# Kernel tuning notes

Measured on AMD Instinct MI355X. Metric: run time of the kernel, lower is better.

## Reference

```python
import jax, jax.numpy as jnp
import numpy as np

N = 50000
E = 800000
F_IN = 128
H = 64
C = 10
BN_EPS = 1e-5


def _glorot(key, shape):
    fan_in = shape[0]
    return jax.random.normal(key, shape, dtype=jnp.float32) / jnp.sqrt(jnp.float32(fan_in))


def setup_inputs() -> dict:
    key = jax.random.key(0)
    ks = jax.random.split(key, 16)
    inp = {
        "x": jax.random.normal(ks[0], (N, F_IN), dtype=jnp.float32),
        "edge_index": jax.random.randint(ks[1], (2, E), 0, N, dtype=jnp.int64),
    }
    # GINConv layer params: eps (train_eps=True, init 0), 2-layer MLP, BN affine
    dims = [(F_IN, H), (H, H), (H, H)]
    for i, (din, dout) in enumerate(dims, start=1):
        k1, k2 = jax.random.split(ks[1 + i], 2)
        inp[f"eps{i}"] = jnp.float32(0.0)
        inp[f"w{i}a"] = _glorot(k1, (din, H))
        inp[f"b{i}a"] = jnp.zeros((H,), jnp.float32)
        inp[f"w{i}b"] = _glorot(k2, (H, H))
        inp[f"b{i}b"] = jnp.zeros((H,), jnp.float32)
        inp[f"g{i}"] = jnp.ones((H,), jnp.float32)
        inp[f"be{i}"] = jnp.zeros((H,), jnp.float32)
    inp["lin_w"] = _glorot(ks[10], (H, C))
    inp["lin_b"] = jnp.zeros((C,), jnp.float32)
    return inp


def _gin_conv(x, src, dst, eps, wa, ba, wb, bb, g, be):
    # sum-aggregate neighbor features: scatter-add x[src] into dst rows
    agg = jax.ops.segment_sum(x[src], dst, num_segments=N)
    h = (1.0 + eps) * x + agg
    # MLP: Linear-ReLU-Linear-ReLU-BatchNorm1d (training-mode batch stats)
    h = jax.nn.relu(h @ wa + ba)
    h = jax.nn.relu(h @ wb + bb)
    mean = jnp.mean(h, axis=0)
    var = jnp.var(h, axis=0)
    return (h - mean) * jax.lax.rsqrt(var + BN_EPS) * g + be


def reference(x, edge_index,
              eps1, w1a, b1a, w1b, b1b, g1, be1,
              eps2, w2a, b2a, w2b, b2b, g2, be2,
              eps3, w3a, b3a, w3b, b3b, g3, be3,
              lin_w, lin_b):
    src, dst = edge_index[0], edge_index[1]
    h = jax.nn.relu(_gin_conv(x, src, dst, eps1, w1a, b1a, w1b, b1b, g1, be1))
    h = jax.nn.relu(_gin_conv(h, src, dst, eps2, w2a, b2a, w2b, b2b, g2, be2))
    h = jax.nn.relu(_gin_conv(h, src, dst, eps3, w3a, b3a, w3b, b3b, g3, be3))
    return h @ lin_w + lin_b
```

## Files before the change

kernel.cpp:

```cpp
#include <hip/hip_runtime.h>
#include <hip/hip_fp16.h>

#define NN 50000
#define NGROUP 3125
#define NCHUNK 391
#define CHCAP 3072
#define SLAB 8192
#define NREP 8
#define BN_EPS 1e-5f

typedef unsigned int uint;
typedef unsigned short ushort;
typedef _Float16 half8 __attribute__((ext_vector_type(8)));
typedef _Float16 half2t __attribute__((ext_vector_type(2)));
typedef float floatx4 __attribute__((ext_vector_type(4)));

__device__ __forceinline__ int aswz(int slot) { return slot ^ ((slot >> 4) & 7); }

__device__ __forceinline__ float h_lo(uint u) {
    return __half2float(__ushort_as_half((ushort)(u & 0xFFFFu)));
}
__device__ __forceinline__ float h_hi(uint u) {
    return __half2float(__ushort_as_half((ushort)(u >> 16)));
}
__device__ __forceinline__ void unpack8(uint4 v, float* f) {
    f[0] = h_lo(v.x); f[1] = h_hi(v.x);
    f[2] = h_lo(v.y); f[3] = h_hi(v.y);
    f[4] = h_lo(v.z); f[5] = h_hi(v.z);
    f[6] = h_lo(v.w); f[7] = h_hi(v.w);
}
__device__ __forceinline__ uint pkadd(uint a, uint b) {
    half2t x = __builtin_bit_cast(half2t, a);
    half2t y = __builtin_bit_cast(half2t, b);
    half2t r = x + y;
    return __builtin_bit_cast(uint, r);
}
__device__ __forceinline__ void pkadd4(uint4& a, uint4 b) {
    a.x = pkadd(a.x, b.x); a.y = pkadd(a.y, b.y);
    a.z = pkadd(a.z, b.z); a.w = pkadd(a.w, b.w);
}

__global__ __launch_bounds__(256) void sortA_kernel(
    const int* __restrict__ ei, int* __restrict__ gcur,
    uint* __restrict__ bucket, int E)
{
    __shared__ int s_hist[NCHUNK];
    __shared__ int s_offs[NCHUNK];
    __shared__ int s_cur[NCHUNK];
    __shared__ int s_gb[NCHUNK];
    __shared__ int s_scanA[512], s_scanB[512];
    __shared__ uint s_sorted[SLAB];

    const int tid  = threadIdx.x;
    const int base = blockIdx.x * SLAB;
    const int cnt  = min(SLAB, E - base);

    for (int i = tid; i < NCHUNK; i += 256) s_hist[i] = 0;
    __syncthreads();

    uint pk[SLAB / 256];
    int nloc = 0;
    for (int i = tid; i < cnt; i += 256) {
        int src = ei[base + i];
        int dst = ei[E + base + i];
        int c = dst >> 7;
        pk[nloc++] = (uint)src | ((uint)(dst & 127) << 16) | ((uint)c << 23);
        atomicAdd(&s_hist[c], 1);
    }
    __syncthreads();
    for (int i = tid; i < 512; i += 256) s_scanA[i] = (i < NCHUNK) ? s_hist[i] : 0;
    __syncthreads();
    int* sa = s_scanA; int* sb = s_scanB;
    for (int off = 1; off < 512; off <<= 1) {
        for (int i = tid; i < 512; i += 256)
            sb[i] = sa[i] + ((i >= off) ? sa[i - off] : 0);
        __syncthreads();
        int* t = sa; sa = sb; sb = t;
    }
    for (int i = tid; i < NCHUNK; i += 256) {
        int excl = sa[i] - s_hist[i];
        s_offs[i] = excl;
        s_cur[i]  = excl;
    }
    __syncthreads();
    for (int k = 0; k < nloc; k++) {
        int c = pk[k] >> 23;
        int pos = atomicAdd(&s_cur[c], 1);
        s_sorted[pos] = pk[k];
    }
    __syncthreads();
    for (int c = tid; c < NCHUNK; c += 256) {
        int n = s_hist[c];
        s_gb[c] = n ? atomicAdd(&gcur[c], n) : 0;
    }
    __syncthreads();
    for (int i = tid; i < cnt; i += 256) {
        uint v = s_sorted[i];
        int c = v >> 23;
        int li = i - s_offs[c];
        bucket[(size_t)c * CHCAP + s_gb[c] + li] = v;
    }
}

__global__ __launch_bounds__(256) void fillB_kernel(
    const uint* __restrict__ bucket, const int* __restrict__ gcur,
    int* __restrict__ rowPtr, int* __restrict__ csr_src)
{
    __shared__ int s_hist[128];
    __shared__ int s_excl[128];
    __shared__ int s_cur[128];
    __shared__ int s_ws[4];
    __shared__ int s_base;
    const int c = blockIdx.x;
    const int tid = threadIdx.x;
    const int cnt = gcur[c];
    const int row0 = c * 128;

    int part = 0;
    for (int i = tid; i < c; i += 256) part += gcur[i];
    #pragma unroll
    for (int off = 32; off >= 1; off >>= 1) part += __shfl_down(part, off, 64);
    if ((tid & 63) == 0) s_ws[tid >> 6] = part;
    if (tid < 128) s_hist[tid] = 0;
    __syncthreads();
    if (tid == 0) s_base = s_ws[0] + s_ws[1] + s_ws[2] + s_ws[3];
    __syncthreads();
    const int base = s_base;
    if (tid == 0 && c == NCHUNK - 1) rowPtr[NN] = base + cnt;

    for (int i = tid; i < cnt; i += 256) {
        uint v = bucket[(size_t)c * CHCAP + i];
        atomicAdd(&s_hist[(v >> 16) & 127], 1);
    }
    __syncthreads();
    if (tid < 128) {
        int lane = tid & 63;
        int v = s_hist[tid];
        int incl = v;
        #pragma unroll
        for (int off = 1; off < 64; off <<= 1) {
            int t = __shfl_up(incl, off, 64);
            if (lane >= off) incl += t;
        }
        s_excl[tid] = incl - v;
    }
    __syncthreads();
    if (tid < 128) {
        int excl = s_excl[tid];
        if (tid >= 64) excl += s_excl[63] + s_hist[63];
        s_cur[tid] = excl;
        int row = row0 + tid;
        if (row < NN) rowPtr[row] = base + excl;
    }
    __syncthreads();
    for (int i = tid; i < cnt; i += 256) {
        uint v = bucket[(size_t)c * CHCAP + i];
        int dl  = (v >> 16) & 127;
        int src = v & 0xFFFFu;
        int ofs = atomicAdd(&s_cur[dl], 1);
        csr_src[base + ofs] = src;
    }
}

template<int FIN, bool APPLY>
__global__ __launch_bounds__(256, 4) void proj_kernel(
    const void* __restrict__ in_v,
    const float* __restrict__ stats_in, const float* __restrict__ g_in,
    const float* __restrict__ be_in,
    const float* __restrict__ wa,
    const float* __restrict__ wb_src, _Float16* __restrict__ wbh_out,
    ushort* __restrict__ y_out)
{
    constexpr int KC = FIN / 32;
    __shared__ __align__(16) _Float16 s_B[FIN * 64];
    __shared__ __align__(16) _Float16 s_Y[4][1024];

    const int tid = threadIdx.x, w = tid >> 6, lane = tid & 63;
    const int q = lane >> 4, mm = lane & 15;

    if (blockIdx.x < 8) {
        for (int t = tid; t < 512; t += 256) {
            int i = blockIdx.x * 512 + t;
            int j = i & 7, l = (i >> 3) & 63, tt = i >> 9;
            int kc = tt >> 2, nt = tt & 3;
            int k = kc * 32 + (l >> 4) * 8 + j;
            int n = nt * 16 + (l & 15);
            wbh_out[i] = (_Float16)wb_src[k * 64 + n];
        }
    }

    for (int i = tid; i < FIN * 64; i += 256) {
        int j = i & 7, l = (i >> 3) & 63, t = i >> 9;
        int kc = t >> 2, nt = t & 3;
        int k = kc * 32 + (l >> 4) * 8 + j;
        int n = nt * 16 + (l & 15);
        s_B[i] = (_Float16)wa[k * 64 + n];
    }

    float scv[2][8], shv[2][8];
    if (APPLY) {
        #pragma unroll
        for (int kc = 0; kc < 2; kc++)
            #pragma unroll
            for (int j = 0; j < 8; j++) {
                int c = kc * 32 + q * 8 + j;
                float s0 = 0.f, s1 = 0.f;
                #pragma unroll
                for (int r = 0; r < NREP; r++) {
                    s0 += stats_in[r * 128 + c];
                    s1 += stats_in[r * 128 + 64 + c];
                }
                float mean = s0 * (1.0f / NN);
                float var  = s1 * (1.0f / NN) - mean * mean;
                float rstd = rsqrtf(var + BN_EPS);
                float s    = rstd * g_in[c];
                scv[kc][j] = s;
                shv[kc][j] = be_in[c] - mean * s;
            }
    }
    __syncthreads();

    int g = blockIdx.x * 4 + w;
    if (g >= NGROUP) return;
    const int row = g * 16 + mm;

    half8 af[KC];
    if (FIN == 128) {
        const float* xin = (const float*)in_v;
        #pragma unroll
        for (int kc = 0; kc < KC; kc++) {
            const float* p = xin + (size_t)row * 128 + kc * 32 + q * 8;
            float4 a = *(const float4*)p;
            float4 b = *(const float4*)(p + 4);
            half8 hv;
            hv[0] = (_Float16)a.x; hv[1] = (_Float16)a.y;
            hv[2] = (_Float16)a.z; hv[3] = (_Float16)a.w;
            hv[4] = (_Float16)b.x; hv[5] = (_Float16)b.y;
            hv[6] = (_Float16)b.z; hv[7] = (_Float16)b.w;
            af[kc] = hv;
        }
    } else {
        const ushort* hin = (const ushort*)in_v;
        #pragma unroll
        for (int kc = 0; kc < KC; kc++) {
            uint4 vv = *(const uint4*)(hin + (size_t)row * 64 + kc * 32 + q * 8);
            float f[8]; unpack8(vv, f);
            half8 hv;
            #pragma unroll
            for (int j = 0; j < 8; j++) {
                float z = APPLY ? fmaxf(fmaf(f[j], scv[kc][j], shv[kc][j]), 0.0f) : f[j];
                hv[j] = (_Float16)z;
            }
            af[kc] = hv;
        }
    }

    floatx4 acc[4] = {};
    #pragma unroll
    for (int nt = 0; nt < 4; nt++)
        #pragma unroll
        for (int kc = 0; kc < KC; kc++) {
            half8 bf = *(const half8*)(s_B + ((size_t)(kc * 4 + nt) * 64 + lane) * 8);
            acc[nt] = __builtin_amdgcn_mfma_f32_16x16x32_f16(af[kc], bf, acc[nt], 0, 0, 0);
        }

    _Float16* s_Yw = &s_Y[w][0];
    #pragma unroll
    for (int nt = 0; nt < 4; nt++)
        #pragma unroll
        for (int r = 0; r < 4; r++)
            s_Yw[(q * 4 + r) * 64 + nt * 16 + mm] = (_Float16)acc[nt][r];
    half8 t0 = *(const half8*)(s_Yw + lane * 8);
    half8 t1 = *(const half8*)(s_Yw + 512 + lane * 8);
    half8* dst = (half8*)((_Float16*)y_out + (size_t)g * 1024);
    dst[lane] = t0;
    dst[64 + lane] = t1;
}

__global__ __launch_bounds__(512, 4) void gin_gather_kernel(
    const ushort* __restrict__ y,
    const int* __restrict__ rowPtr, const int* __restrict__ csr_src,
    const float* __restrict__ eps_p, const float* __restrict__ ba,
    const _Float16* __restrict__ wbh, const float* __restrict__ bb,
    ushort* __restrict__ h_out, float* __restrict__ stats_out)
{
    __shared__ __align__(16) _Float16 s_B2[64 * 64];
    __shared__ __align__(16) _Float16 s_A[2][1024];
    __shared__ float s_red[2][128];

    const int tid = threadIdx.x, w = tid >> 6, lane = tid & 63;
    const int gl = w >> 2;
    const int m  = (w & 3) * 4;
    const int cc = lane & 7, gph = lane >> 3;
    const int q = lane >> 4, mm = lane & 15;

    ((half8*)s_B2)[tid] = ((const half8*)wbh)[tid];
    if (tid < 256) ((float*)s_red)[tid] = 0.0f;

    const float eps1 = 1.0f + eps_p[0];
    __syncthreads();

    const uint4* y4 = (const uint4*)y;
    const int g = blockIdx.x * 2 + gl;

    if (g < NGROUP) {
        const int row0 = g * 16;
        _Float16* s_Aw = &s_A[gl][0];

        int e[4], en[4], s[4];
        uint4 v[4];
        uint4 pk[4];
        #pragma unroll
        for (int i = 0; i < 4; i++) {
            int row = row0 + m + i;
            e[i] = rowPtr[row] + gph;
            en[i] = rowPtr[row + 1];
            pk[i].x = pk[i].y = pk[i].z = pk[i].w = 0u;
        }
        #pragma unroll
        for (int i = 0; i < 4; i++) s[i] = (e[i] < en[i]) ? csr_src[e[i]] : -1;
        #pragma unroll
        for (int i = 0; i < 4; i++) if (s[i] >= 0) v[i] = y4[(size_t)s[i] * 8 + cc];

        int mx = max(max(s[0], s[1]), max(s[2], s[3]));
        while (mx >= 0) {
            int n[4]; uint4 p[4];
            #pragma unroll
            for (int i = 0; i < 4; i++) {
                n[i] = -1;
                if (s[i] >= 0) { e[i] += 8; n[i] = (e[i] < en[i]) ? csr_src[e[i]] : -1; }
            }
            #pragma unroll
            for (int i = 0; i < 4; i++) if (n[i] >= 0) p[i] = y4[(size_t)n[i] * 8 + cc];
            #pragma unroll
            for (int i = 0; i < 4; i++) {
                if (s[i] >= 0) pkadd4(pk[i], v[i]);
                s[i] = n[i]; v[i] = p[i];
            }
            mx = max(max(s[0], s[1]), max(s[2], s[3]));
        }

        #pragma unroll
        for (int i = 0; i < 4; i++) {
            float a[8];
            unpack8(pk[i], a);
            if (gph == 0) {
                uint4 sv = y4[(size_t)(row0 + m + i) * 8 + cc];
                float f[8]; unpack8(sv, f);
                #pragma unroll
                for (int j = 0; j < 8; j++) a[j] = fmaf(eps1, f[j], a[j]);
            }
            #pragma unroll
            for (int off = 8; off < 64; off <<= 1)
                #pragma unroll
                for (int j = 0; j < 8; j++)
                    a[j] += __shfl_xor(a[j], off, 64);
            if (gph == 0) {
                half8 hv;
                #pragma unroll
                for (int j = 0; j < 8; j++)
                    hv[j] = (_Float16)fmaxf(a[j] + ba[8 * cc + j], 0.0f);
                int slot = (cc >> 2) * 64 + (cc & 3) * 16 + (m + i);
                *(half8*)(s_Aw + (size_t)aswz(slot) * 8) = hv;
            }
        }
    }
    __syncthreads();

    if ((w & 3) == 0 && g < NGROUP) {
        const int row0 = g * 16;
        _Float16* s_Aw = &s_A[gl][0];
        float bbv[4];
        #pragma unroll
        for (int nt = 0; nt < 4; nt++) bbv[nt] = bb[nt * 16 + mm];

        half8 af2[2];
        #pragma unroll
        for (int kc = 0; kc < 2; kc++)
            af2[kc] = *(const half8*)(s_Aw + (size_t)aswz(kc * 64 + lane) * 8);
        floatx4 acc2[4] = {};
        #pragma unroll
        for (int nt = 0; nt < 4; nt++)
            #pragma unroll
            for (int kc = 0; kc < 2; kc++) {
                half8 bf = *(const half8*)(s_B2 + ((size_t)(kc * 4 + nt) * 64 + lane) * 8);
                acc2[nt] = __builtin_amdgcn_mfma_f32_16x16x32_f16(af2[kc], bf, acc2[nt], 0, 0, 0);
            }

        float bn_s[4] = {0.f, 0.f, 0.f, 0.f};
        float bn_q[4] = {0.f, 0.f, 0.f, 0.f};
        #pragma unroll
        for (int nt = 0; nt < 4; nt++)
            #pragma unroll
            for (int r = 0; r < 4; r++) {
                float val = fmaxf(acc2[nt][r] + bbv[nt], 0.0f);
                bn_s[nt] += val;
                bn_q[nt] += val * val;
                s_Aw[(q * 4 + r) * 64 + nt * 16 + mm] = (_Float16)val;
            }
        half8 t0 = *(const half8*)(s_Aw + lane * 8);
        half8 t1 = *(const half8*)(s_Aw + 512 + lane * 8);
        half8* dst = (half8*)((_Float16*)h_out + (size_t)row0 * 64);
        dst[lane] = t0;
        dst[64 + lane] = t1;

        #pragma unroll
        for (int nt = 0; nt < 4; nt++) {
            bn_s[nt] += __shfl_xor(bn_s[nt], 16, 64);
            bn_s[nt] += __shfl_xor(bn_s[nt], 32, 64);
            bn_q[nt] += __shfl_xor(bn_q[nt], 16, 64);
            bn_q[nt] += __shfl_xor(bn_q[nt], 32, 64);
        }
        if (lane < 16) {
            #pragma unroll
            for (int nt = 0; nt < 4; nt++) {
                s_red[gl][nt * 16 + lane]      = bn_s[nt];
                s_red[gl][64 + nt * 16 + lane] = bn_q[nt];
            }
        }
    }
    __syncthreads();
    if (w == 0) {
        float* srep = stats_out + (size_t)(blockIdx.x & (NREP - 1)) * 128;
        atomicAdd(&srep[lane],      s_red[0][lane]      + s_red[1][lane]);
        atomicAdd(&srep[64 + lane], s_red[0][64 + lane] + s_red[1][64 + lane]);
    }
}

__global__ __launch_bounds__(256) void final_linear_kernel(
    const ushort* __restrict__ h, const float* __restrict__ stats,
    const float* __restrict__ g, const float* __restrict__ be,
    const float* __restrict__ w, const float* __restrict__ b,
    float* __restrict__ out)
{
    __shared__ float s_w[640];
    __shared__ float s_b[10];
    __shared__ float s_scale[64];
    __shared__ float s_shift[64];
    for (int i = threadIdx.x; i < 640; i += 256) s_w[i] = w[i];
    if (threadIdx.x < 10) s_b[threadIdx.x] = b[threadIdx.x];
    if (threadIdx.x < 64) {
        int c = threadIdx.x;
        float s0 = 0.f, s1 = 0.f;
        #pragma unroll
        for (int r = 0; r < NREP; r++) {
            s0 += stats[r * 128 + c];
            s1 += stats[r * 128 + 64 + c];
        }
        float mean = s0 * (1.0f / NN);
        float var  = s1 * (1.0f / NN) - mean * mean;
        float rstd = rsqrtf(var + BN_EPS);
        float s    = rstd * g[c];
        s_scale[c] = s;
        s_shift[c] = be[c] - mean * s;
    }
    __syncthreads();
    int row = blockIdx.x * 256 + threadIdx.x;
    if (row >= NN) return;
    float acc[10];
    #pragma unroll
    for (int c = 0; c < 10; c++) acc[c] = s_b[c];
    const uint4* hr = (const uint4*)(h + (size_t)row * 64);
    #pragma unroll
    for (int ch = 0; ch < 8; ch++) {
        uint4 v = hr[ch];
        float f[8]; unpack8(v, f);
        #pragma unroll
        for (int j = 0; j < 8; j++) {
            int k = ch * 8 + j;
            float val = fmaxf(fmaf(f[j], s_scale[k], s_shift[k]), 0.0f);
            #pragma unroll
            for (int c = 0; c < 10; c++) acc[c] = fmaf(val, s_w[k * 10 + c], acc[c]);
        }
    }
    #pragma unroll
    for (int c = 0; c < 10; c++) out[row * 10 + c] = acc[c];
}

extern "C" void kernel_launch(void* const* d_in, const int* in_sizes, int n_in,
                              void* d_out, int out_size, void* d_ws, size_t ws_size,
                              hipStream_t stream)
{
    const float* x  = (const float*)d_in[0];
    const int*   ei = (const int*)d_in[1];
    const int E = in_sizes[1] / 2;

    const float* eps[3]; const float* wa[3]; const float* ba[3];
    const float* wb[3];  const float* bb[3]; const float* g[3]; const float* be[3];
    for (int i = 0; i < 3; i++) {
        int base = 2 + 7 * i;
        eps[i] = (const float*)d_in[base + 0];
        wa[i]  = (const float*)d_in[base + 1];
        ba[i]  = (const float*)d_in[base + 2];
        wb[i]  = (const float*)d_in[base + 3];
        bb[i]  = (const float*)d_in[base + 4];
        g[i]   = (const float*)d_in[base + 5];
        be[i]  = (const float*)d_in[base + 6];
    }
    const float* lin_w = (const float*)d_in[23];
    const float* lin_b = (const float*)d_in[24];
    float* out = (float*)d_out;

    char*  base   = (char*)d_ws;
    int*   gcur   = (int*)base;
    float* stats  = (float*)(gcur + 512);
    int*   rowPtr = (int*)(stats + 3 * NREP * 128);
    uint*  bucket = (uint*)(rowPtr + NN + 1);
    int*   csrsrc = (int*)(bucket + (size_t)NCHUNK * CHCAP);
    size_t hoff   = (char*)(csrsrc + E) - base;
    _Float16* wbh = (_Float16*)(base + ((hoff + 15) & ~(size_t)15));
    ushort* yb    = (ushort*)(wbh + 4096);
    ushort* hA    = yb + (size_t)NN * 64;
    ushort* hB    = hA + (size_t)NN * 64;

    hipMemsetAsync(gcur, 0, (512 + 3 * NREP * 128) * sizeof(int), stream);
    sortA_kernel<<<(E + SLAB - 1) / SLAB, 256, 0, stream>>>(ei, gcur, bucket, E);
    fillB_kernel<<<NCHUNK, 256, 0, stream>>>(bucket, gcur, rowPtr, csrsrc);

    const int PB = (NGROUP + 3) / 4;
    const int GB = (NGROUP + 1) / 2;

    proj_kernel<128, false><<<PB, 256, 0, stream>>>(
        x, nullptr, nullptr, nullptr, wa[0], wb[0], wbh, yb);
    gin_gather_kernel<<<GB, 512, 0, stream>>>(
        yb, rowPtr, csrsrc, eps[0], ba[0], wbh, bb[0], hA, stats);
    proj_kernel<64, true><<<PB, 256, 0, stream>>>(
        hA, stats, g[0], be[0], wa[1], wb[1], wbh, yb);
    gin_gather_kernel<<<GB, 512, 0, stream>>>(
        yb, rowPtr, csrsrc, eps[1], ba[1], wbh, bb[1], hB, stats + NREP * 128);
    proj_kernel<64, true><<<PB, 256, 0, stream>>>(
        hB, stats + NREP * 128, g[1], be[1], wa[2], wb[2], wbh, yb);
    gin_gather_kernel<<<GB, 512, 0, stream>>>(
        yb, rowPtr, csrsrc, eps[2], ba[2], wbh, bb[2], hA, stats + 2 * NREP * 128);
    final_linear_kernel<<<(NN + 255) / 256, 256, 0, stream>>>(
        hA, stats + 2 * NREP * 128, g[2], be[2], lin_w, lin_b, out);
}
```

Measured before the change: 322.6 us.

## Give each gather wave a full 16-row group and shrink sort slab

```diff
diff --git a/kernel.cpp b/kernel.cpp
--- a/kernel.cpp
+++ b/kernel.cpp
@@ -5,7 +5,7 @@
 #define NGROUP 3125
 #define NCHUNK 391
 #define CHCAP 3072
-#define SLAB 8192
+#define SLAB 2048
 #define NREP 8
 #define BN_EPS 1e-5f
 
@@ -57,15 +57,9 @@
 
     for (int i = tid; i < NCHUNK; i += 256) s_hist[i] = 0;
     __syncthreads();
-
-    uint pk[SLAB / 256];
-    int nloc = 0;
     for (int i = tid; i < cnt; i += 256) {
-        int src = ei[base + i];
         int dst = ei[E + base + i];
-        int c = dst >> 7;
-        pk[nloc++] = (uint)src | ((uint)(dst & 127) << 16) | ((uint)c << 23);
-        atomicAdd(&s_hist[c], 1);
+        atomicAdd(&s_hist[dst >> 7], 1);
     }
     __syncthreads();
     for (int i = tid; i < 512; i += 256) s_scanA[i] = (i < NCHUNK) ? s_hist[i] : 0;
@@ -83,10 +77,13 @@
         s_cur[i]  = excl;
     }
     __syncthreads();
-    for (int k = 0; k < nloc; k++) {
-        int c = pk[k] >> 23;
+    for (int i = tid; i < cnt; i += 256) {
+        int src = ei[base + i];
+        int dst = ei[E + base + i];
+        int c = dst >> 7;
+        uint v = (uint)src | ((uint)(dst & 127) << 16) | ((uint)c << 23);
         int pos = atomicAdd(&s_cur[c], 1);
-        s_sorted[pos] = pk[k];
+        s_sorted[pos] = v;
     }
     __syncthreads();
     for (int c = tid; c < NCHUNK; c += 256) {
@@ -280,96 +277,92 @@
 __global__ __launch_bounds__(512, 4) void gin_gather_kernel(
     const ushort* __restrict__ y,
     const int* __restrict__ rowPtr, const int* __restrict__ csr_src,
-    const float* __restrict__ eps_p, const float* __restrict__ ba,
-    const _Float16* __restrict__ wbh, const float* __restrict__ bb,
+    const float* __restrict__ eps_p, const _Float16* __restrict__ wbh,
+    const float* __restrict__ ba, const float* __restrict__ bb,
     ushort* __restrict__ h_out, float* __restrict__ stats_out)
 {
     __shared__ __align__(16) _Float16 s_B2[64 * 64];
-    __shared__ __align__(16) _Float16 s_A[2][1024];
-    __shared__ float s_red[2][128];
+    __shared__ __align__(16) _Float16 s_A[8][1024];
+    __shared__ float s_red[8][64];
 
     const int tid = threadIdx.x, w = tid >> 6, lane = tid & 63;
-    const int gl = w >> 2;
-    const int m  = (w & 3) * 4;
     const int cc = lane & 7, gph = lane >> 3;
     const int q = lane >> 4, mm = lane & 15;
 
     ((half8*)s_B2)[tid] = ((const half8*)wbh)[tid];
-    if (tid < 256) ((float*)s_red)[tid] = 0.0f;
 
     const float eps1 = 1.0f + eps_p[0];
     __syncthreads();
 
+    float bn_s[4] = {0.f, 0.f, 0.f, 0.f};
+    float bn_q[4] = {0.f, 0.f, 0.f, 0.f};
     const uint4* y4 = (const uint4*)y;
-    const int g = blockIdx.x * 2 + gl;
+    const int g = blockIdx.x * 8 + w;
 
     if (g < NGROUP) {
         const int row0 = g * 16;
-        _Float16* s_Aw = &s_A[gl][0];
-
-        int e[4], en[4], s[4];
-        uint4 v[4];
-        uint4 pk[4];
-        #pragma unroll
-        for (int i = 0; i < 4; i++) {
-            int row = row0 + m + i;
-            e[i] = rowPtr[row] + gph;
-            en[i] = rowPtr[row + 1];
-            pk[i].x = pk[i].y = pk[i].z = pk[i].w = 0u;
-        }
-        #pragma unroll
-        for (int i = 0; i < 4; i++) s[i] = (e[i] < en[i]) ? csr_src[e[i]] : -1;
-        #pragma unroll
-        for (int i = 0; i < 4; i++) if (s[i] >= 0) v[i] = y4[(size_t)s[i] * 8 + cc];
-
-        int mx = max(max(s[0], s[1]), max(s[2], s[3]));
-        while (mx >= 0) {
-            int n[4]; uint4 p[4];
+        _Float16* s_Aw = &s_A[w][0];
+
+        for (int m = 0; m < 16; m += 4) {
+            int e[4], en[4], s[4];
+            uint4 v[4];
+            uint4 pk[4];
             #pragma unroll
             for (int i = 0; i < 4; i++) {
-                n[i] = -1;
-                if (s[i] >= 0) { e[i] += 8; n[i] = (e[i] < en[i]) ? csr_src[e[i]] : -1; }
-            }
-            #pragma unroll
-            for (int i = 0; i < 4; i++) if (n[i] >= 0) p[i] = y4[(size_t)n[i] * 8 + cc];
+                int row = row0 + m + i;
+                e[i] = rowPtr[row] + gph;
+                en[i] = rowPtr[row + 1];
+                pk[i].x = pk[i].y = pk[i].z = pk[i].w = 0u;
+            }
+            #pragma unroll
+            for (int i = 0; i < 4; i++) s[i] = (e[i] < en[i]) ? csr_src[e[i]] : -1;
+            #pragma unroll
+            for (int i = 0; i < 4; i++) if (s[i] >= 0) v[i] = y4[(size_t)s[i] * 8 + cc];
+
+            int mx = max(max(s[0], s[1]), max(s[2], s[3]));
+            while (mx >= 0) {
+                int n[4]; uint4 p[4];
+                #pragma unroll
+                for (int i = 0; i < 4; i++) {
+                    n[i] = -1;
+                    if (s[i] >= 0) { e[i] += 8; n[i] = (e[i] < en[i]) ? csr_src[e[i]] : -1; }
+                }
+                #pragma unroll
+                for (int i = 0; i < 4; i++) if (n[i] >= 0) p[i] = y4[(size_t)n[i] * 8 + cc];
+                #pragma unroll
+                for (int i = 0; i < 4; i++) {
+                    if (s[i] >= 0) pkadd4(pk[i], v[i]);
+                    s[i] = n[i]; v[i] = p[i];
+                }
+                mx = max(max(s[0], s[1]), max(s[2], s[3]));
+            }
+
             #pragma unroll
             for (int i = 0; i < 4; i++) {
-                if (s[i] >= 0) pkadd4(pk[i], v[i]);
-                s[i] = n[i]; v[i] = p[i];
-            }
-            mx = max(max(s[0], s[1]), max(s[2], s[3]));
-        }
-
-        #pragma unroll
-        for (int i = 0; i < 4; i++) {
-            float a[8];
-            unpack8(pk[i], a);
-            if (gph == 0) {
-                uint4 sv = y4[(size_t)(row0 + m + i) * 8 + cc];
-                float f[8]; unpack8(sv, f);
+                float a[8];
+                unpack8(pk[i], a);
+                if (gph == 0) {
+                    uint4 sv = y4[(size_t)(row0 + m + i) * 8 + cc];
+                    float f[8]; unpack8(sv, f);
+                    #pragma unroll
+                    for (int j = 0; j < 8; j++) a[j] = fmaf(eps1, f[j], a[j]);
+                }
                 #pragma unroll
-                for (int j = 0; j < 8; j++) a[j] = fmaf(eps1, f[j], a[j]);
-            }
-            #pragma unroll
-            for (int off = 8; off < 64; off <<= 1)
-                #pragma unroll
-                for (int j = 0; j < 8; j++)
-                    a[j] += __shfl_xor(a[j], off, 64);
-            if (gph == 0) {
-                half8 hv;
-                #pragma unroll
-                for (int j = 0; j < 8; j++)
-                    hv[j] = (_Float16)fmaxf(a[j] + ba[8 * cc + j], 0.0f);
-                int slot = (cc >> 2) * 64 + (cc & 3) * 16 + (m + i);
-                *(half8*)(s_Aw + (size_t)aswz(slot) * 8) = hv;
-            }
-        }
-    }
-    __syncthreads();
-
-    if ((w & 3) == 0 && g < NGROUP) {
-        const int row0 = g * 16;
-        _Float16* s_Aw = &s_A[gl][0];
+                for (int off = 8; off < 64; off <<= 1)
+                    #pragma unroll
+                    for (int j = 0; j < 8; j++)
+                        a[j] += __shfl_xor(a[j], off, 64);
+                if (gph == 0) {
+                    half8 hv;
+                    #pragma unroll
+                    for (int j = 0; j < 8; j++)
+                        hv[j] = (_Float16)fmaxf(a[j] + ba[8 * cc + j], 0.0f);
+                    int slot = (cc >> 2) * 64 + (cc & 3) * 16 + (m + i);
+                    *(half8*)(s_Aw + (size_t)aswz(slot) * 8) = hv;
+                }
+            }
+        }
+
         float bbv[4];
         #pragma unroll
         for (int nt = 0; nt < 4; nt++) bbv[nt] = bb[nt * 16 + mm];
@@ -387,8 +380,6 @@
                 acc2[nt] = __builtin_amdgcn_mfma_f32_16x16x32_f16(af2[kc], bf, acc2[nt], 0, 0, 0);
             }
 
-        float bn_s[4] = {0.f, 0.f, 0.f, 0.f};
-        float bn_q[4] = {0.f, 0.f, 0.f, 0.f};
         #pragma unroll
         for (int nt = 0; nt < 4; nt++)
             #pragma unroll
@@ -403,27 +394,38 @@
         half8* dst = (half8*)((_Float16*)h_out + (size_t)row0 * 64);
         dst[lane] = t0;
         dst[64 + lane] = t1;
-
-        #pragma unroll
-        for (int nt = 0; nt < 4; nt++) {
-            bn_s[nt] += __shfl_xor(bn_s[nt], 16, 64);
-            bn_s[nt] += __shfl_xor(bn_s[nt], 32, 64);
-            bn_q[nt] += __shfl_xor(bn_q[nt], 16, 64);
-            bn_q[nt] += __shfl_xor(bn_q[nt], 32, 64);
-        }
-        if (lane < 16) {
-            #pragma unroll
-            for (int nt = 0; nt < 4; nt++) {
-                s_red[gl][nt * 16 + lane]      = bn_s[nt];
-                s_red[gl][64 + nt * 16 + lane] = bn_q[nt];
-            }
-        }
+    }
+
+    #pragma unroll
+    for (int nt = 0; nt < 4; nt++) {
+        bn_s[nt] += __shfl_xor(bn_s[nt], 16, 64);
+        bn_s[nt] += __shfl_xor(bn_s[nt], 32, 64);
+        bn_q[nt] += __shfl_xor(bn_q[nt], 16, 64);
+        bn_q[nt] += __shfl_xor(bn_q[nt], 32, 64);
+    }
+    __syncthreads();
+    if (lane < 16) {
+        #pragma unroll
+        for (int nt = 0; nt < 4; nt++) s_red[w][nt * 16 + lane] = bn_s[nt];
     }
     __syncthreads();
     if (w == 0) {
-        float* srep = stats_out + (size_t)(blockIdx.x & (NREP - 1)) * 128;
-        atomicAdd(&srep[lane],      s_red[0][lane]      + s_red[1][lane]);
-        atomicAdd(&srep[64 + lane], s_red[0][64 + lane] + s_red[1][64 + lane]);
+        float s = 0;
+        #pragma unroll
+        for (int j = 0; j < 8; j++) s += s_red[j][lane];
+        atomicAdd(&stats_out[(size_t)(blockIdx.x & (NREP - 1)) * 128 + lane], s);
+    }
+    __syncthreads();
+    if (lane < 16) {
+        #pragma unroll
+        for (int nt = 0; nt < 4; nt++) s_red[w][nt * 16 + lane] = bn_q[nt];
+    }
+    __syncthreads();
+    if (w == 0) {
+        float s = 0;
+        #pragma unroll
+        for (int j = 0; j < 8; j++) s += s_red[j][lane];
+        atomicAdd(&stats_out[(size_t)(blockIdx.x & (NREP - 1)) * 128 + 64 + lane], s);
     }
 }
 
@@ -518,20 +520,20 @@
     fillB_kernel<<<NCHUNK, 256, 0, stream>>>(bucket, gcur, rowPtr, csrsrc);
 
     const int PB = (NGROUP + 3) / 4;
-    const int GB = (NGROUP + 1) / 2;
+    const int GB = (NGROUP + 7) / 8;
 
     proj_kernel<128, false><<<PB, 256, 0, stream>>>(
         x, nullptr, nullptr, nullptr, wa[0], wb[0], wbh, yb);
     gin_gather_kernel<<<GB, 512, 0, stream>>>(
-        yb, rowPtr, csrsrc, eps[0], ba[0], wbh, bb[0], hA, stats);
+        yb, rowPtr, csrsrc, eps[0], wbh, ba[0], bb[0], hA, stats);
     proj_kernel<64, true><<<PB, 256, 0, stream>>>(
         hA, stats, g[0], be[0], wa[1], wb[1], wbh, yb);
     gin_gather_kernel<<<GB, 512, 0, stream>>>(
-        yb, rowPtr, csrsrc, eps[1], ba[1], wbh, bb[1], hB, stats + NREP * 128);
+        yb, rowPtr, csrsrc, eps[1], wbh, ba[1], bb[1], hB, stats + NREP * 128);
     proj_kernel<64, true><<<PB, 256, 0, stream>>>(
         hB, stats + NREP * 128, g[1], be[1], wa[2], wb[2], wbh, yb);
     gin_gather_kernel<<<GB, 512, 0, stream>>>(
-        yb, rowPtr, csrsrc, eps[2], ba[2], wbh, bb[2], hA, stats + 2 * NREP * 128);
+        yb, rowPtr, csrsrc, eps[2], wbh, ba[2], bb[2], hA, stats + 2 * NREP * 128);
     final_linear_kernel<<<(NN + 255) / 256, 256, 0, stream>>>(
         hA, stats + 2 * NREP * 128, g[2], be[2], lin_w, lin_b, out);
 }
```

Result: faster. 314.5 us (-2.5%).
